# Optimization experiments

Hardware: AMD Instinct MI355X
Metric: run time of the kernel (lower is better)

Reference implementation:

```python
import jax, jax.numpy as jnp
import numpy as np

N_W = 96  # n_workers
N_F = 96  # n_firms


def setup_inputs() -> dict:
    key = jax.random.key(0)
    kw, kf, kr = jax.random.split(key, 3)
    # Each worker ranks the n_firms+1 options (firms + unmatch) with a random permutation,
    # encoded as a one-hot (n_firms+1, n_firms+1) matrix: W[i, j, k] = 1 iff firm j is at rank k.
    pw = jax.vmap(lambda k: jax.random.permutation(k, N_F + 1))(jax.random.split(kw, N_W))
    W = jnp.eye(N_F + 1, dtype=jnp.float32)[pw]                  # (N_W, N_F+1, N_F+1)
    pf = jax.vmap(lambda k: jax.random.permutation(k, N_W + 1))(jax.random.split(kf, N_F))
    F = jnp.eye(N_W + 1, dtype=jnp.float32)[pf]                  # (N_F, N_W+1, N_W+1)
    # R: permutation (dictatorship order) matrix over all workers+firms; column r is one-hot
    # on the agent that dictates in round r.
    perm = jax.random.permutation(kr, N_W + N_F)
    R = jnp.eye(N_W + N_F, dtype=jnp.float32)[perm]              # (N_W+N_F, N_W+N_F)
    return {"W": W, "F": F, "R": R}


def _triangle_window(x):
    # TriangleWindowFunction.forward: x on (0,1], 2-x on (1,2], 0 elsewhere (clamped at 0).
    return jnp.clip(jnp.where(x > 1.0, 2.0 - x, jnp.where(x > 0.0, x, 0.0)), 0.0)


def _find_counterpart(P):
    # first available (rank-first) choice indicator, then map rank -> agent via P.
    first_j = _triangle_window(jnp.cumsum(jnp.sum(P, axis=0)))
    return P @ first_j[:, None]                                  # (n+1, 1)


def _forward(W, F, R):
    n_w, n_f = W.shape[0], F.shape[0]
    dt = W.dtype
    gate_w = jnp.concatenate([jnp.ones((n_f, 1), dt), jnp.zeros((1, 1), dt)])  # zero out unmatch row
    gate_f = jnp.concatenate([jnp.ones((n_w, 1), dt), jnp.zeros((1, 1), dt)])
    zero1 = jnp.zeros((1,), dt)

    def step(carry, ds):
        Wc, Fc, M = carry
        d_w, d_f = ds                                            # (n_w,), (n_f,)
        P_w = jnp.einsum('wij,w->ij', Wc, d_w)                   # dictator-worker's ranking
        P_f = jnp.einsum('fij,f->ij', Fc, d_f)
        c_w = _find_counterpart(P_w)                             # (n_f+1, 1)
        c_f = _find_counterpart(P_f)                             # (n_w+1, 1)
        dw1 = jnp.concatenate([d_w, zero1])                      # (n_w+1,)
        df1 = jnp.concatenate([d_f, zero1])                      # (n_f+1,)
        # matching += M_w + M_f.T
        M = M + dw1[:, None] * c_w[:, 0][None, :] + c_f * df1[None, :]
        # ranking_masks_for_workers[r] has row i = -d_f[i] (0 on unmatch row): equals -df1[:,None].
        # matching_mask_for_workers = -(c_w * gate_w) broadcast across columns.
        Wn = jnp.clip(Wc - c_w * gate_w - df1[:, None], 0.0) * (1.0 - c_f)[:n_w, :, None]
        Fn = jnp.clip(Fc - c_f * gate_f - dw1[:, None], 0.0) * (1.0 - c_w)[:n_f, :, None]
        return (Wn, Fn, M), None

    xs = (R[:n_w].T, R[n_w:].T)                                  # per-round dictator indicators
    M0 = jnp.zeros((n_w + 1, n_f + 1), dt)
    (_, _, M), _ = jax.lax.scan(step, (W, F, M0), xs)
    return M


def reference(W, F, R):
    return _forward(W, F, R)
```

## Files before the change

kernel.cpp:

```cpp
#include <hip/hip_runtime.h>
#include <hip/hip_bf16.h>
#include <stdint.h>

#define N_W 96
#define NAG 192
#define NP1 97
#define W_ELEMS (N_W * NP1 * NP1)
#define R_ELEMS (NAG * NAG)
#define WB ((W_ELEMS / 4 + 255) / 256)
#define RB ((R_ELEMS / 4 + 255) / 256)

__global__ __launch_bounds__(256) void decode_kernel(
    const float* __restrict__ W, const float* __restrict__ F,
    const float* __restrict__ R,
    short* __restrict__ ps, short* __restrict__ ord) {
    int b = blockIdx.x;
    if (b < 2 * WB) {
        const float* src = (b < WB) ? W : F;
        int abase = (b < WB) ? 0 : N_W;
        int i4 = (b - ((b < WB) ? 0 : WB)) * 256 + threadIdx.x;
        if (i4 < W_ELEMS / 4) {
            float4 v = ((const float4*)src)[i4];
            int base = i4 * 4;
            #pragma unroll
            for (int u = 0; u < 4; ++u) {
                float x = (u == 0) ? v.x : (u == 1) ? v.y : (u == 2) ? v.z : v.w;
                if (x > 0.5f) {
                    int idx = base + u;
                    int a = idx / (NP1 * NP1);
                    int rem = idx - a * (NP1 * NP1);
                    int j = rem / NP1;
                    int k = rem - j * NP1;
                    int slot = (k < 64) ? (2 * k) : (2 * (k - 64) + 1);
                    ps[(abase + a) * 128 + slot] = (short)j;
                }
            }
        }
    } else {
        int i4 = (b - 2 * WB) * 256 + threadIdx.x;
        if (i4 < R_ELEMS / 4) {
            float4 v = ((const float4*)R)[i4];
            int base = i4 * 4;
            #pragma unroll
            for (int u = 0; u < 4; ++u) {
                float x = (u == 0) ? v.x : (u == 1) ? v.y : (u == 2) ? v.z : v.w;
                if (x > 0.5f) {
                    int idx = base + u;
                    int a = idx / NAG;
                    int r = idx - a * NAG;
                    ord[r] = (short)a;
                }
            }
        }
    }
}

__global__ __launch_bounds__(256, 1) void sd_kernel(
    const uint32_t* __restrict__ pk_g, const short* __restrict__ ord_g,
    float* __restrict__ out) {
    __shared__ __align__(16) uint32_t s_pko[NAG * 64 + 64];
    __shared__ uint32_t s_match[NAG];

    const int t = threadIdx.x;
    const unsigned short* og = (const unsigned short*)ord_g;

    for (int idx = t; idx < NAG * 16; idx += 256) {
        int r = idx >> 4, q = idx & 15;
        int a = (int)og[r];
        ((uint4*)s_pko)[idx] = ((const uint4*)(pk_g + (a << 6)))[q];
    }
    __syncthreads();

    if (t < 64) {
        uint32_t ov0 = og[t], ov1 = og[64 + t], ov2 = og[128 + t];
        uint64_t rWlo = 0, rWhi = 0, rFlo = 0, rFhi = 0;
        uint32_t c0 = 0xFFFFFFFFu, c1 = 0xFFFFFFFFu, c2 = 0xFFFFFFFFu;
        uint32_t Pc = s_pko[t];

        auto runseg = [&](uint32_t ordv, uint32_t& cellv, int segbase) {
            #pragma clang loop unroll(disable)
            for (int rr = 0; rr < 64; ++rr) {
                const int r = segbase + rr;
                uint32_t Pn = s_pko[((r + 1) << 6) + t];
                int a = __builtin_amdgcn_readlane((int)ordv, rr);
                uint32_t j1 = Pc & 0xFFFFu, j2 = Pc >> 16;
                uint32_t s1 = j1 & 63u, s2 = j2 & 63u;
                bool h1 = j1 >= 64u, h2 = j2 >= 64u;
                if (a < 96) {
                    uint64_t own = (a >= 64) ? rWhi : rWlo;
                    uint64_t sb = 1ull << (a & 63);
                    if (a >= 64) rWhi |= sb; else rWlo |= sb;
                    if (((own >> (a & 63)) & 1ull) == 0ull) {
                        uint32_t b1 = (h1 ? (uint32_t)(rFhi >> s1)
                                          : (uint32_t)(rFlo >> s1)) & 1u;
                        unsigned long long m1 = __ballot(b1 == 0u);
                        uint32_t js;
                        if (m1 != 0ull) {
                            int k = __ffsll(m1) - 1;
                            js = ((uint32_t)__builtin_amdgcn_readlane((int)Pc, k)) & 0xFFFFu;
                        } else {
                            uint32_t b2 = (h2 ? (uint32_t)(rFhi >> s2)
                                              : (uint32_t)(rFlo >> s2)) & 1u;
                            unsigned long long m2 = __ballot(b2 == 0u) & 0x1FFFFFFFFull;
                            int k = __ffsll(m2) - 1;
                            js = ((uint32_t)__builtin_amdgcn_readlane((int)Pc, k)) >> 16;
                        }
                        uint64_t cb = 1ull << (js & 63u);
                        rFlo |= (js < 64u) ? cb : 0ull;
                        rFhi |= (js >= 64u && js < 96u) ? cb : 0ull;
                        uint32_t cellu = (uint32_t)(a * NP1) + js;
                        cellv = (t == rr) ? cellu : cellv;
                    }
                } else {
                    int aa = a - 96;
                    uint64_t own = (aa >= 64) ? rFhi : rFlo;
                    uint64_t sb = 1ull << (aa & 63);
                    if (aa >= 64) rFhi |= sb; else rFlo |= sb;
                    if (((own >> (aa & 63)) & 1ull) == 0ull) {
                        uint32_t b1 = (h1 ? (uint32_t)(rWhi >> s1)
                                          : (uint32_t)(rWlo >> s1)) & 1u;
                        unsigned long long m1 = __ballot(b1 == 0u);
                        uint32_t js;
                        if (m1 != 0ull) {
                            int k = __ffsll(m1) - 1;
                            js = ((uint32_t)__builtin_amdgcn_readlane((int)Pc, k)) & 0xFFFFu;
                        } else {
                            uint32_t b2 = (h2 ? (uint32_t)(rWhi >> s2)
                                              : (uint32_t)(rWlo >> s2)) & 1u;
                            unsigned long long m2 = __ballot(b2 == 0u) & 0x1FFFFFFFFull;
                            int k = __ffsll(m2) - 1;
                            js = ((uint32_t)__builtin_amdgcn_readlane((int)Pc, k)) >> 16;
                        }
                        uint64_t cb = 1ull << (js & 63u);
                        rWlo |= (js < 64u) ? cb : 0ull;
                        rWhi |= (js >= 64u && js < 96u) ? cb : 0ull;
                        uint32_t cellu = js * (uint32_t)NP1 + (uint32_t)aa;
                        cellv = (t == rr) ? cellu : cellv;
                    }
                }
                Pc = Pn;
            }
        };
        runseg(ov0, c0, 0);
        runseg(ov1, c1, 64);
        runseg(ov2, c2, 128);
        s_match[t] = c0; s_match[64 + t] = c1; s_match[128 + t] = c2;
    } else {
        for (int i = t - 64; i < 2352; i += 192)
            ((float4*)out)[i] = make_float4(0.f, 0.f, 0.f, 0.f);
        if (t == 64) out[9408] = 0.f;
    }
    __syncthreads();
    if (t < NAG) {
        uint32_t c = s_match[t];
        if (c != 0xFFFFFFFFu) out[c] = 1.0f;
    }
}

extern "C" void kernel_launch(void* const* d_in, const int* in_sizes, int n_in,
                              void* d_out, int out_size, void* d_ws, size_t ws_size,
                              hipStream_t stream) {
    const float* W = (const float*)d_in[0];
    const float* F = (const float*)d_in[1];
    const float* R = (const float*)d_in[2];
    float* out = (float*)d_out;

    uint32_t* packed = (uint32_t*)d_ws;
    short* ord = (short*)((char*)d_ws + NAG * 64 * 4);

    decode_kernel<<<2 * WB + RB, 256, 0, stream>>>(W, F, R, (short*)packed, ord);
    sd_kernel<<<1, 256, 0, stream>>>(packed, ord, out);
}
```

Before: 46.12 us.

## Precompute dictator round per agent to drop own-turn bits from serial loop

Decode now records each agent's dictation round (inverse order). While staging preference lists into shared memory, entries naming counterparts who already dictated earlier are replaced with a sentinel. This means the serial loop no longer has to set the dictator's own bit each round. Only the matched-state bitmasks are kept, with high words pre-seeded so the sentinel reads as taken, which shortens the per-round dependency chain in the single-wave serial loop. The cost is extra work in the parallel staging phase plus an extra workspace array and shared loads.

```diff
diff --git a/kernel.cpp b/kernel.cpp
--- a/kernel.cpp
+++ b/kernel.cpp
@@ -13,7 +13,7 @@
 __global__ __launch_bounds__(256) void decode_kernel(
     const float* __restrict__ W, const float* __restrict__ F,
     const float* __restrict__ R,
-    short* __restrict__ ps, short* __restrict__ ord) {
+    short* __restrict__ ps, short* __restrict__ ord, short* __restrict__ td) {
     int b = blockIdx.x;
     if (b < 2 * WB) {
         const float* src = (b < WB) ? W : F;
@@ -49,6 +49,7 @@
                     int a = idx / NAG;
                     int r = idx - a * NAG;
                     ord[r] = (short)a;
+                    td[a] = (short)r;
                 }
             }
         }
@@ -57,93 +58,111 @@
 
 __global__ __launch_bounds__(256, 1) void sd_kernel(
     const uint32_t* __restrict__ pk_g, const short* __restrict__ ord_g,
-    float* __restrict__ out) {
+    const short* __restrict__ td_g, float* __restrict__ out) {
     __shared__ __align__(16) uint32_t s_pko[NAG * 64 + 64];
     __shared__ uint32_t s_match[NAG];
+    __shared__ unsigned short s_og[NAG];
+    __shared__ unsigned short s_td[NAG];
 
     const int t = threadIdx.x;
-    const unsigned short* og = (const unsigned short*)ord_g;
+    if (t < NAG) {
+        s_og[t] = ((const unsigned short*)ord_g)[t];
+        s_td[t] = ((const unsigned short*)td_g)[t];
+    }
+    __syncthreads();
 
     for (int idx = t; idx < NAG * 16; idx += 256) {
         int r = idx >> 4, q = idx & 15;
-        int a = (int)og[r];
-        ((uint4*)s_pko)[idx] = ((const uint4*)(pk_g + (a << 6)))[q];
+        int a = (int)s_og[r];
+        uint4 w = ((const uint4*)(pk_g + (a << 6)))[q];
+        int opp = (a < 96) ? 96 : 0;
+        uint32_t* pw = (uint32_t*)&w;
+        #pragma unroll
+        for (int u = 0; u < 4; ++u) {
+            uint32_t x = pw[u];
+            uint32_t j1 = x & 0xFFFFu, j2 = x >> 16;
+            if (j1 < 96u && (int)s_td[opp + j1] < r) j1 = 97u;
+            if (j2 < 96u && (int)s_td[opp + j2] < r) j2 = 97u;
+            pw[u] = j1 | (j2 << 16);
+        }
+        ((uint4*)s_pko)[idx] = w;
     }
     __syncthreads();
 
     if (t < 64) {
-        uint32_t ov0 = og[t], ov1 = og[64 + t], ov2 = og[128 + t];
-        uint64_t rWlo = 0, rWhi = 0, rFlo = 0, rFhi = 0;
+        uint32_t ov0 = s_og[t], ov1 = s_og[64 + t], ov2 = s_og[128 + t];
+        uint64_t chW = 0, chWh = (1ull << 33), chF = 0, chFh = (1ull << 33);
         uint32_t c0 = 0xFFFFFFFFu, c1 = 0xFFFFFFFFu, c2 = 0xFFFFFFFFu;
         uint32_t Pc = s_pko[t];
+        uint32_t j1 = Pc & 0xFFFFu;
 
-        auto runseg = [&](uint32_t ordv, uint32_t& cellv, int segbase) {
+        auto SEG = [&](uint32_t ordv, uint32_t& cv, int segbase) {
             #pragma clang loop unroll(disable)
             for (int rr = 0; rr < 64; ++rr) {
                 const int r = segbase + rr;
                 uint32_t Pn = s_pko[((r + 1) << 6) + t];
                 int a = __builtin_amdgcn_readlane((int)ordv, rr);
-                uint32_t j1 = Pc & 0xFFFFu, j2 = Pc >> 16;
-                uint32_t s1 = j1 & 63u, s2 = j2 & 63u;
-                bool h1 = j1 >= 64u, h2 = j2 >= 64u;
                 if (a < 96) {
-                    uint64_t own = (a >= 64) ? rWhi : rWlo;
-                    uint64_t sb = 1ull << (a & 63);
-                    if (a >= 64) rWhi |= sb; else rWlo |= sb;
+                    uint64_t own = (a < 64) ? chW : chWh;
                     if (((own >> (a & 63)) & 1ull) == 0ull) {
-                        uint32_t b1 = (h1 ? (uint32_t)(rFhi >> s1)
-                                          : (uint32_t)(rFlo >> s1)) & 1u;
-                        unsigned long long m1 = __ballot(b1 == 0u);
+                        uint32_t t0 = (uint32_t)(chF >> (j1 & 63u));
+                        uint32_t t1 = (uint32_t)(chFh >> (j1 & 63u));
+                        uint32_t bit = (j1 < 64u) ? t0 : t1;
+                        unsigned long long m1 = __ballot((bit & 1u) == 0u);
                         uint32_t js;
                         if (m1 != 0ull) {
                             int k = __ffsll(m1) - 1;
                             js = ((uint32_t)__builtin_amdgcn_readlane((int)Pc, k)) & 0xFFFFu;
                         } else {
-                            uint32_t b2 = (h2 ? (uint32_t)(rFhi >> s2)
-                                              : (uint32_t)(rFlo >> s2)) & 1u;
-                            unsigned long long m2 = __ballot(b2 == 0u) & 0x1FFFFFFFFull;
+                            uint32_t j2 = Pc >> 16;
+                            uint32_t u0 = (uint32_t)(chF >> (j2 & 63u));
+                            uint32_t u1 = (uint32_t)(chFh >> (j2 & 63u));
+                            uint32_t b2 = (j2 < 64u) ? u0 : u1;
+                            unsigned long long m2 = __ballot((b2 & 1u) == 0u) & 0x1FFFFFFFFull;
                             int k = __ffsll(m2) - 1;
                             js = ((uint32_t)__builtin_amdgcn_readlane((int)Pc, k)) >> 16;
                         }
-                        uint64_t cb = 1ull << (js & 63u);
-                        rFlo |= (js < 64u) ? cb : 0ull;
-                        rFhi |= (js >= 64u && js < 96u) ? cb : 0ull;
-                        uint32_t cellu = (uint32_t)(a * NP1) + js;
-                        cellv = (t == rr) ? cellu : cellv;
+                        if (js < 96u) {
+                            if (js < 64u) chF |= 1ull << js; else chFh |= 1ull << (js & 63u);
+                        }
+                        uint32_t cell = (uint32_t)(a * NP1) + js;
+                        cv = (t == (uint32_t)rr) ? cell : cv;
                     }
                 } else {
                     int aa = a - 96;
-                    uint64_t own = (aa >= 64) ? rFhi : rFlo;
-                    uint64_t sb = 1ull << (aa & 63);
-                    if (aa >= 64) rFhi |= sb; else rFlo |= sb;
+                    uint64_t own = (aa < 64) ? chF : chFh;
                     if (((own >> (aa & 63)) & 1ull) == 0ull) {
-                        uint32_t b1 = (h1 ? (uint32_t)(rWhi >> s1)
-                                          : (uint32_t)(rWlo >> s1)) & 1u;
-                        unsigned long long m1 = __ballot(b1 == 0u);
+                        uint32_t t0 = (uint32_t)(chW >> (j1 & 63u));
+                        uint32_t t1 = (uint32_t)(chWh >> (j1 & 63u));
+                        uint32_t bit = (j1 < 64u) ? t0 : t1;
+                        unsigned long long m1 = __ballot((bit & 1u) == 0u);
                         uint32_t js;
                         if (m1 != 0ull) {
                             int k = __ffsll(m1) - 1;
                             js = ((uint32_t)__builtin_amdgcn_readlane((int)Pc, k)) & 0xFFFFu;
                         } else {
-                            uint32_t b2 = (h2 ? (uint32_t)(rWhi >> s2)
-                                              : (uint32_t)(rWlo >> s2)) & 1u;
-                            unsigned long long m2 = __ballot(b2 == 0u) & 0x1FFFFFFFFull;
+                            uint32_t j2 = Pc >> 16;
+                            uint32_t u0 = (uint32_t)(chW >> (j2 & 63u));
+                            uint32_t u1 = (uint32_t)(chWh >> (j2 & 63u));
+                            uint32_t b2 = (j2 < 64u) ? u0 : u1;
+                            unsigned long long m2 = __ballot((b2 & 1u) == 0u) & 0x1FFFFFFFFull;
                             int k = __ffsll(m2) - 1;
                             js = ((uint32_t)__builtin_amdgcn_readlane((int)Pc, k)) >> 16;
                         }
-                        uint64_t cb = 1ull << (js & 63u);
-                        rWlo |= (js < 64u) ? cb : 0ull;
-                        rWhi |= (js >= 64u && js < 96u) ? cb : 0ull;
-                        uint32_t cellu = js * (uint32_t)NP1 + (uint32_t)aa;
-                        cellv = (t == rr) ? cellu : cellv;
+                        if (js < 96u) {
+                            if (js < 64u) chW |= 1ull << js; else chWh |= 1ull << (js & 63u);
+                        }
+                        uint32_t cell = js * (uint32_t)NP1 + (uint32_t)aa;
+                        cv = (t == (uint32_t)rr) ? cell : cv;
                     }
                 }
                 Pc = Pn;
+                j1 = Pn & 0xFFFFu;
             }
         };
-        runseg(ov0, c0, 0);
-        runseg(ov1, c1, 64);
-        runseg(ov2, c2, 128);
+        SEG(ov0, c0, 0);
+        SEG(ov1, c1, 64);
+        SEG(ov2, c2, 128);
         s_match[t] = c0; s_match[64 + t] = c1; s_match[128 + t] = c2;
     } else {
         for (int i = t - 64; i < 2352; i += 192)
@@ -167,7 +186,8 @@
 
     uint32_t* packed = (uint32_t*)d_ws;
     short* ord = (short*)((char*)d_ws + NAG * 64 * 4);
+    short* td  = (short*)((char*)d_ws + NAG * 64 * 4 + NAG * 2);
 
-    decode_kernel<<<2 * WB + RB, 256, 0, stream>>>(W, F, R, (short*)packed, ord);
-    sd_kernel<<<1, 256, 0, stream>>>(packed, ord, out);
+    decode_kernel<<<2 * WB + RB, 256, 0, stream>>>(W, F, R, (short*)packed, ord, td);
+    sd_kernel<<<1, 256, 0, stream>>>(packed, ord, td, out);
 }
```

Result: no change. 46.89 us (+1.7%).
